# Optimization experiments

Hardware: AMD Instinct MI355X
Metric: run time of the kernel (lower is better)

Reference implementation:

```python
import jax, jax.numpy as jnp
import numpy as np

N_QUBITS = 10
N_GEN = 4
Q_DEPTH = 6
BATCH = 1024


def _cz_chain_diag(n):
    # Diagonal of the CZ chain CZ(0,1) CZ(1,2) ... CZ(n-2,n-1):
    # phase (-1)^(# adjacent 1-1 pairs) per computational basis state.
    idx = np.arange(2 ** n)
    bits = (idx[:, None] >> np.arange(n - 1, -1, -1)) & 1  # wire 0 = most significant (PennyLane)
    pairs = (bits[:, :-1] & bits[:, 1:]).sum(axis=1)
    return ((-1.0) ** pairs).astype(np.float32).reshape((2,) * n)

_CZ = jnp.asarray(_cz_chain_diag(N_QUBITS))


def _ry(t):
    c = jnp.cos(0.5 * t)
    s = jnp.sin(0.5 * t)
    return jnp.stack([jnp.stack([c, -s]), jnp.stack([s, c])]).astype(jnp.complex64)


def _rx(t):
    c = jnp.cos(0.5 * t).astype(jnp.complex64)
    js = (1j * jnp.sin(0.5 * t)).astype(jnp.complex64)
    return jnp.stack([jnp.stack([c, -js]), jnp.stack([-js, c])])


def _apply_1q(state, gate, wire):
    # state: (2,)*n complex statevector; apply 2x2 gate on `wire`.
    state = jnp.moveaxis(state, wire, -1)
    state = jnp.einsum('...j,ij->...i', state, gate)
    return jnp.moveaxis(state, -1, wire)


def _circuit(noise_s, weights, cz):
    # noise_s: (n_qubits,), weights: (q_depth, n_qubits)
    n = noise_s.shape[0]
    state = jnp.zeros((2,) * n, jnp.complex64).at[(0,) * n].set(1.0)
    for q in range(n):
        state = _apply_1q(state, _ry(noise_s[q]), q)
        state = _apply_1q(state, _rx(noise_s[q]), q)

    def layer(st, w):
        for q in range(n):
            st = _apply_1q(st, _ry(w[q]), q)
        return st * cz, None

    state, _ = jax.lax.scan(layer, state, weights)
    # <X_q> = Re <psi| X_q |psi>; X_q flips the q-th wire.
    return jnp.stack([jnp.real(jnp.vdot(state, jnp.flip(state, axis=q))) for q in range(n)])


def setup_inputs() -> dict:
    key = jax.random.key(0)
    k1, k2 = jax.random.split(key)
    noise = jax.random.normal(k1, (BATCH, N_QUBITS), dtype=jnp.float32)
    q_params = jax.random.uniform(k2, (N_GEN, Q_DEPTH, N_QUBITS), dtype=jnp.float32)  # q_delta=1.0 * rand
    return {"noise": noise, "q_params": q_params}


def reference(noise, q_params):
    per_sample = lambda ns, w: _circuit(ns, w, _CZ)
    per_gen = jax.vmap(lambda w: jax.vmap(lambda ns: per_sample(ns, w))(noise))(q_params)  # (G, B, n)
    out = jnp.transpose(per_gen, (1, 0, 2)).reshape(noise.shape[0], N_GEN * N_QUBITS)
    return out.astype(jnp.float32)
```

## Files before the change

### kernel.cpp

```cpp
#include <hip/hip_runtime.h>

#define NQ 10
#define NG 4
#define QD 6
#define NBATCH 1024
#define WPB 4


template<int CTRL, int RM, int BM, bool BC>
__device__ __forceinline__ float dppmov(float x) {
    return __int_as_float(__builtin_amdgcn_update_dpp(
        0, __float_as_int(x), CTRL, RM, BM, BC));
}

__device__ __forceinline__ float pxor1 (float x){ return dppmov<0xB1,0xF,0xF,false>(x); }
__device__ __forceinline__ float pxor2 (float x){ return dppmov<0x4E,0xF,0xF,false>(x); }
__device__ __forceinline__ float pxor4 (float x){
    return dppmov<0x1B,0xF,0xF,false>(dppmov<0x141,0xF,0xF,false>(x));
}
__device__ __forceinline__ float pxor8 (float x){
    return dppmov<0x141,0xF,0xF,false>(dppmov<0x140,0xF,0xF,false>(x));
}
__device__ __forceinline__ float pxor16(float x){ return __shfl_xor(x, 16, 64); }
__device__ __forceinline__ float pxor32(float x){ return __shfl_xor(x, 32, 64); }

struct PX1  { static __device__ __forceinline__ float f(float x){ return pxor1(x); } };
struct PX2  { static __device__ __forceinline__ float f(float x){ return pxor2(x); } };
struct PX4  { static __device__ __forceinline__ float f(float x){ return pxor4(x); } };
struct PX8  { static __device__ __forceinline__ float f(float x){ return pxor8(x); } };
struct PX16 { static __device__ __forceinline__ float f(float x){ return pxor16(x); } };
struct PX32 { static __device__ __forceinline__ float f(float x){ return pxor32(x); } };

__device__ __forceinline__ float wave_reduce(float x) {
    x += dppmov<0x111,0xF,0xF,true >(x);
    x += dppmov<0x112,0xF,0xF,true >(x);
    x += dppmov<0x114,0xF,0xF,true >(x);
    x += dppmov<0x118,0xF,0xF,true >(x);
    x += dppmov<0x142,0xA,0xF,false>(x);
    x += dppmov<0x143,0xC,0xF,false>(x);
    return __int_as_float(__builtin_amdgcn_readlane(__float_as_int(x), 63));
}

template<class PF, int LM>
__device__ __forceinline__ void cross_rot(float (&ar)[16], float (&ai)[16],
                                          float c, float s, int lane) {
    const float sgn = (lane & LM) ? s : -s;
#pragma unroll
    for (int j = 0; j < 16; ++j) {
        float pa = PF::f(ar[j]);
        float pb = PF::f(ai[j]);
        ar[j] = c * ar[j] + sgn * pa;
        ai[j] = c * ai[j] + sgn * pb;
    }
}

template<int M>
__device__ __forceinline__ void intra_rot(float (&ar)[16], float (&ai)[16],
                                          float c, float s) {
#pragma unroll
    for (int j = 0; j < 16; ++j) {
        if ((j & M) == 0) {
            const int k = j | M;
            float a0 = ar[j], a1 = ar[k];
            ar[j] = c * a0 - s * a1;
            ar[k] = s * a0 + c * a1;
            float b0 = ai[j], b1 = ai[k];
            ai[j] = c * b0 - s * b1;
            ai[k] = s * b0 + c * b1;
        }
    }
}

template<class PF>
__device__ __forceinline__ float cross_exp(const float (&ar)[16], const float (&ai)[16]) {
    float sum = 0.f;
#pragma unroll
    for (int j = 0; j < 16; ++j)
        sum += ar[j] * PF::f(ar[j]) + ai[j] * PF::f(ai[j]);
    return sum;
}

template<int M>
__device__ __forceinline__ float intra_exp(const float (&ar)[16], const float (&ai)[16]) {
    float sum = 0.f;
#pragma unroll
    for (int j = 0; j < 16; ++j)
        sum += ar[j] * ar[j ^ M] + ai[j] * ai[j ^ M];
    return sum;
}

__global__ __launch_bounds__(64 * WPB) void qsim_kernel(
    const float* __restrict__ noise,
    const float* __restrict__ qp,
    float* __restrict__ out)
{
    const int wave = threadIdx.x >> 6;
    const int lane = threadIdx.x & 63;
    const int g    = blockIdx.x & 3;
    const int b    = (blockIdx.x >> 2) * WPB + wave;

    float nc[NQ], ns[NQ];
#pragma unroll
    for (int q = 0; q < NQ; ++q) {
        float t = 0.5f * noise[b * NQ + q];
        __sincosf(t, &ns[q], &nc[q]);
    }

    float ar[16], ai[16];
    float hr = 1.f, hi = 0.f;
#pragma unroll
    for (int p = 4; p <= 9; ++p) {
        const int q = NQ - 1 - p;
        const int bit = (lane >> (p - 4)) & 1;
        float cc = nc[q], ss = ns[q];
        float gr, gi;
        if (bit) { gr = cc * ss; gi = -gr; }
        else     { gr = cc * cc; gi = -ss * ss; }
        float tr = hr * gr - hi * gi;
        float ti = hr * gi + hi * gr;
        hr = tr; hi = ti;
    }
#pragma unroll
    for (int j = 0; j < 16; ++j) {
        float r = hr, im = hi;
#pragma unroll
        for (int p = 0; p < 4; ++p) {
            const int q = NQ - 1 - p;
            float cc = nc[q], ss = ns[q];
            float gr, gi;
            if ((j >> p) & 1) { gr = cc * ss; gi = -gr; }
            else              { gr = cc * cc; gi = -ss * ss; }
            float tr = r * gr - im * gi;
            float ti = r * gi + im * gr;
            r = tr; im = ti;
        }
        ar[j] = r; ai[j] = im;
    }

    float czs[16];
#pragma unroll
    for (int j = 0; j < 16; ++j) {
        unsigned i = ((unsigned)lane << 4) | (unsigned)j;
        czs[j] = (__popc(i & (i >> 1)) & 1) ? -1.f : 1.f;
    }

    const float* w = qp + g * (QD * NQ);
#pragma unroll 1
    for (int l = 0; l < QD; ++l) {
        float c[NQ], sn[NQ];
#pragma unroll
        for (int q = 0; q < NQ; ++q)
            __sincosf(0.5f * w[l * NQ + q], &sn[q], &c[q]);

        cross_rot<PX32,32>(ar, ai, c[0], sn[0], lane);
        cross_rot<PX16,16>(ar, ai, c[1], sn[1], lane);
        cross_rot<PX8 , 8>(ar, ai, c[2], sn[2], lane);
        cross_rot<PX4 , 4>(ar, ai, c[3], sn[3], lane);
        cross_rot<PX2 , 2>(ar, ai, c[4], sn[4], lane);
        cross_rot<PX1 , 1>(ar, ai, c[5], sn[5], lane);
        intra_rot<8>(ar, ai, c[6], sn[6]);
        intra_rot<4>(ar, ai, c[7], sn[7]);
        intra_rot<2>(ar, ai, c[8], sn[8]);
        intra_rot<1>(ar, ai, c[9], sn[9]);

#pragma unroll
        for (int j = 0; j < 16; ++j) { ar[j] *= czs[j]; ai[j] *= czs[j]; }
    }

    float outval = 0.f;
    {
        float s0 = wave_reduce(cross_exp<PX32>(ar, ai)); outval = (lane == 0) ? s0 : outval;
        float s1 = wave_reduce(cross_exp<PX16>(ar, ai)); outval = (lane == 1) ? s1 : outval;
        float s2 = wave_reduce(cross_exp<PX8 >(ar, ai)); outval = (lane == 2) ? s2 : outval;
        float s3 = wave_reduce(cross_exp<PX4 >(ar, ai)); outval = (lane == 3) ? s3 : outval;
        float s4 = wave_reduce(cross_exp<PX2 >(ar, ai)); outval = (lane == 4) ? s4 : outval;
        float s5 = wave_reduce(cross_exp<PX1 >(ar, ai)); outval = (lane == 5) ? s5 : outval;
        float s6 = wave_reduce(intra_exp<8>(ar, ai));    outval = (lane == 6) ? s6 : outval;
        float s7 = wave_reduce(intra_exp<4>(ar, ai));    outval = (lane == 7) ? s7 : outval;
        float s8 = wave_reduce(intra_exp<2>(ar, ai));    outval = (lane == 8) ? s8 : outval;
        float s9 = wave_reduce(intra_exp<1>(ar, ai));    outval = (lane == 9) ? s9 : outval;
    }

    if (lane < NQ)
        out[b * (NG * NQ) + g * NQ + lane] = outval;
}

extern "C" void kernel_launch(void* const* d_in, const int* in_sizes, int n_in,
                              void* d_out, int out_size, void* d_ws, size_t ws_size,
                              hipStream_t stream) {
    const float* noise = (const float*)d_in[0];
    const float* qp    = (const float*)d_in[1];
    float* out = (float*)d_out;

    const int nblocks = (NBATCH * NG) / WPB;
    qsim_kernel<<<nblocks, 64 * WPB, 0, stream>>>(noise, qp, out);
}
```

Baseline: 99.61 us.

## Pack complex amplitudes into float2 vectors, swizzle xor16, factor initial state

Stores each amplitude as a float2 vector so the compiler can emit packed FP32 ops (v_pk_fma/v_pk_mul) for the rotations, CZ phase and expectation sums. The lane-xor-16 exchange moves from a bpermute-based shuffle to ds_swizzle. Initial product-state construction is factored into shared partial products. The aim is fewer VALU instructions per gate, with some risk that the packed code is not generated or that register pressure rises.

```diff
diff --git a/kernel.cpp b/kernel.cpp
--- a/kernel.cpp
+++ b/kernel.cpp
@@ -7,29 +7,32 @@
 #define WPB 4
 
 
+typedef float v2f __attribute__((ext_vector_type(2)));
+
 template<int CTRL, int RM, int BM, bool BC>
 __device__ __forceinline__ float dppmov(float x) {
     return __int_as_float(__builtin_amdgcn_update_dpp(
         0, __float_as_int(x), CTRL, RM, BM, BC));
 }
 
-__device__ __forceinline__ float pxor1 (float x){ return dppmov<0xB1,0xF,0xF,false>(x); }
-__device__ __forceinline__ float pxor2 (float x){ return dppmov<0x4E,0xF,0xF,false>(x); }
-__device__ __forceinline__ float pxor4 (float x){
-    return dppmov<0x1B,0xF,0xF,false>(dppmov<0x141,0xF,0xF,false>(x));
+template<int CTRL>
+__device__ __forceinline__ v2f dpp2(v2f x) {
+    v2f r;
+    r.x = dppmov<CTRL,0xF,0xF,false>(x.x);
+    r.y = dppmov<CTRL,0xF,0xF,false>(x.y);
+    return r;
 }
-__device__ __forceinline__ float pxor8 (float x){
-    return dppmov<0x141,0xF,0xF,false>(dppmov<0x140,0xF,0xF,false>(x));
+
+__device__ __forceinline__ float swz16(float x) {
+    return __int_as_float(__builtin_amdgcn_ds_swizzle(__float_as_int(x), 0x401F));
 }
-__device__ __forceinline__ float pxor16(float x){ return __shfl_xor(x, 16, 64); }
-__device__ __forceinline__ float pxor32(float x){ return __shfl_xor(x, 32, 64); }
 
-struct PX1  { static __device__ __forceinline__ float f(float x){ return pxor1(x); } };
-struct PX2  { static __device__ __forceinline__ float f(float x){ return pxor2(x); } };
-struct PX4  { static __device__ __forceinline__ float f(float x){ return pxor4(x); } };
-struct PX8  { static __device__ __forceinline__ float f(float x){ return pxor8(x); } };
-struct PX16 { static __device__ __forceinline__ float f(float x){ return pxor16(x); } };
-struct PX32 { static __device__ __forceinline__ float f(float x){ return pxor32(x); } };
+struct PX1  { static __device__ __forceinline__ v2f f(v2f x){ return dpp2<0xB1>(x); } };
+struct PX2  { static __device__ __forceinline__ v2f f(v2f x){ return dpp2<0x4E>(x); } };
+struct PX4  { static __device__ __forceinline__ v2f f(v2f x){ return dpp2<0x1B>(dpp2<0x141>(x)); } };
+struct PX8  { static __device__ __forceinline__ v2f f(v2f x){ return dpp2<0x141>(dpp2<0x140>(x)); } };
+struct PX16 { static __device__ __forceinline__ v2f f(v2f x){ v2f r; r.x = swz16(x.x); r.y = swz16(x.y); return r; } };
+struct PX32 { static __device__ __forceinline__ v2f f(v2f x){ v2f r; r.x = __shfl_xor(x.x, 32, 64); r.y = __shfl_xor(x.y, 32, 64); return r; } };
 
 __device__ __forceinline__ float wave_reduce(float x) {
     x += dppmov<0x111,0xF,0xF,true >(x);
@@ -41,52 +44,54 @@
     return __int_as_float(__builtin_amdgcn_readlane(__float_as_int(x), 63));
 }
 
+__device__ __forceinline__ v2f cmul(v2f a, v2f b) {
+    v2f r;
+    r.x = a.x * b.x - a.y * b.y;
+    r.y = a.x * b.y + a.y * b.x;
+    return r;
+}
+
 template<class PF, int LM>
-__device__ __forceinline__ void cross_rot(float (&ar)[16], float (&ai)[16],
-                                          float c, float s, int lane) {
-    const float sgn = (lane & LM) ? s : -s;
+__device__ __forceinline__ void cross_rot(v2f (&s)[16], float c, float sn, int lane) {
+    const float sgn = (lane & LM) ? sn : -sn;
 #pragma unroll
     for (int j = 0; j < 16; ++j) {
-        float pa = PF::f(ar[j]);
-        float pb = PF::f(ai[j]);
-        ar[j] = c * ar[j] + sgn * pa;
-        ai[j] = c * ai[j] + sgn * pb;
+        v2f p = PF::f(s[j]);
+        s[j] = c * s[j] + sgn * p;
     }
 }
 
 template<int M>
-__device__ __forceinline__ void intra_rot(float (&ar)[16], float (&ai)[16],
-                                          float c, float s) {
+__device__ __forceinline__ void intra_rot(v2f (&s)[16], float c, float sn) {
 #pragma unroll
     for (int j = 0; j < 16; ++j) {
         if ((j & M) == 0) {
             const int k = j | M;
-            float a0 = ar[j], a1 = ar[k];
-            ar[j] = c * a0 - s * a1;
-            ar[k] = s * a0 + c * a1;
-            float b0 = ai[j], b1 = ai[k];
-            ai[j] = c * b0 - s * b1;
-            ai[k] = s * b0 + c * b1;
+            v2f v0 = s[j], v1 = s[k];
+            s[j] = c * v0 - sn * v1;
+            s[k] = sn * v0 + c * v1;
         }
     }
 }
 
 template<class PF>
-__device__ __forceinline__ float cross_exp(const float (&ar)[16], const float (&ai)[16]) {
-    float sum = 0.f;
+__device__ __forceinline__ float cross_exp(const v2f (&s)[16]) {
+    v2f acc = {0.f, 0.f};
 #pragma unroll
-    for (int j = 0; j < 16; ++j)
-        sum += ar[j] * PF::f(ar[j]) + ai[j] * PF::f(ai[j]);
-    return sum;
+    for (int j = 0; j < 16; ++j) {
+        v2f p = PF::f(s[j]);
+        acc += s[j] * p;
+    }
+    return acc.x + acc.y;
 }
 
 template<int M>
-__device__ __forceinline__ float intra_exp(const float (&ar)[16], const float (&ai)[16]) {
-    float sum = 0.f;
+__device__ __forceinline__ float intra_exp(const v2f (&s)[16]) {
+    v2f acc = {0.f, 0.f};
 #pragma unroll
     for (int j = 0; j < 16; ++j)
-        sum += ar[j] * ar[j ^ M] + ai[j] * ai[j ^ M];
-    return sum;
+        acc += s[j] * s[j ^ M];
+    return acc.x + acc.y;
 }
 
 __global__ __launch_bounds__(64 * WPB) void qsim_kernel(
@@ -106,35 +111,32 @@
         __sincosf(t, &ns[q], &nc[q]);
     }
 
-    float ar[16], ai[16];
-    float hr = 1.f, hi = 0.f;
+    auto fac = [&](int q, int bit) -> v2f {
+        float cc = nc[q], ss = ns[q];
+        v2f r;
+        if (bit) { r.x = cc * ss; r.y = -r.x; }
+        else     { r.x = cc * cc; r.y = -ss * ss; }
+        return r;
+    };
+
+    v2f h = {1.f, 0.f};
 #pragma unroll
-    for (int p = 4; p <= 9; ++p) {
-        const int q = NQ - 1 - p;
-        const int bit = (lane >> (p - 4)) & 1;
-        float cc = nc[q], ss = ns[q];
-        float gr, gi;
-        if (bit) { gr = cc * ss; gi = -gr; }
-        else     { gr = cc * cc; gi = -ss * ss; }
-        float tr = hr * gr - hi * gi;
-        float ti = hr * gi + hi * gr;
-        hr = tr; hi = ti;
-    }
+    for (int p = 4; p <= 9; ++p)
+        h = cmul(h, fac(NQ - 1 - p, (lane >> (p - 4)) & 1));
+
+    v2f s[16];
+    {
+        v2f t01[4], t23[4];
 #pragma unroll
-    for (int j = 0; j < 16; ++j) {
-        float r = hr, im = hi;
+        for (int a = 0; a < 4; ++a) {
+            t01[a] = cmul(fac(9, a & 1), fac(8, (a >> 1) & 1));
+            t23[a] = cmul(fac(7, a & 1), fac(6, (a >> 1) & 1));
+        }
+        v2f pre[4];
 #pragma unroll
-        for (int p = 0; p < 4; ++p) {
-            const int q = NQ - 1 - p;
-            float cc = nc[q], ss = ns[q];
-            float gr, gi;
-            if ((j >> p) & 1) { gr = cc * ss; gi = -gr; }
-            else              { gr = cc * cc; gi = -ss * ss; }
-            float tr = r * gr - im * gi;
-            float ti = r * gi + im * gr;
-            r = tr; im = ti;
-        }
-        ar[j] = r; ai[j] = im;
+        for (int a = 0; a < 4; ++a) pre[a] = cmul(h, t01[a]);
+#pragma unroll
+        for (int j = 0; j < 16; ++j) s[j] = cmul(pre[j & 3], t23[j >> 2]);
     }
 
     float czs[16];
@@ -152,33 +154,33 @@
         for (int q = 0; q < NQ; ++q)
             __sincosf(0.5f * w[l * NQ + q], &sn[q], &c[q]);
 
-        cross_rot<PX32,32>(ar, ai, c[0], sn[0], lane);
-        cross_rot<PX16,16>(ar, ai, c[1], sn[1], lane);
-        cross_rot<PX8 , 8>(ar, ai, c[2], sn[2], lane);
-        cross_rot<PX4 , 4>(ar, ai, c[3], sn[3], lane);
-        cross_rot<PX2 , 2>(ar, ai, c[4], sn[4], lane);
-        cross_rot<PX1 , 1>(ar, ai, c[5], sn[5], lane);
-        intra_rot<8>(ar, ai, c[6], sn[6]);
-        intra_rot<4>(ar, ai, c[7], sn[7]);
-        intra_rot<2>(ar, ai, c[8], sn[8]);
-        intra_rot<1>(ar, ai, c[9], sn[9]);
+        cross_rot<PX32,32>(s, c[0], sn[0], lane);
+        cross_rot<PX16,16>(s, c[1], sn[1], lane);
+        cross_rot<PX8 , 8>(s, c[2], sn[2], lane);
+        cross_rot<PX4 , 4>(s, c[3], sn[3], lane);
+        cross_rot<PX2 , 2>(s, c[4], sn[4], lane);
+        cross_rot<PX1 , 1>(s, c[5], sn[5], lane);
+        intra_rot<8>(s, c[6], sn[6]);
+        intra_rot<4>(s, c[7], sn[7]);
+        intra_rot<2>(s, c[8], sn[8]);
+        intra_rot<1>(s, c[9], sn[9]);
 
 #pragma unroll
-        for (int j = 0; j < 16; ++j) { ar[j] *= czs[j]; ai[j] *= czs[j]; }
+        for (int j = 0; j < 16; ++j) s[j] *= czs[j];
     }
 
     float outval = 0.f;
     {
-        float s0 = wave_reduce(cross_exp<PX32>(ar, ai)); outval = (lane == 0) ? s0 : outval;
-        float s1 = wave_reduce(cross_exp<PX16>(ar, ai)); outval = (lane == 1) ? s1 : outval;
-        float s2 = wave_reduce(cross_exp<PX8 >(ar, ai)); outval = (lane == 2) ? s2 : outval;
-        float s3 = wave_reduce(cross_exp<PX4 >(ar, ai)); outval = (lane == 3) ? s3 : outval;
-        float s4 = wave_reduce(cross_exp<PX2 >(ar, ai)); outval = (lane == 4) ? s4 : outval;
-        float s5 = wave_reduce(cross_exp<PX1 >(ar, ai)); outval = (lane == 5) ? s5 : outval;
-        float s6 = wave_reduce(intra_exp<8>(ar, ai));    outval = (lane == 6) ? s6 : outval;
-        float s7 = wave_reduce(intra_exp<4>(ar, ai));    outval = (lane == 7) ? s7 : outval;
-        float s8 = wave_reduce(intra_exp<2>(ar, ai));    outval = (lane == 8) ? s8 : outval;
-        float s9 = wave_reduce(intra_exp<1>(ar, ai));    outval = (lane == 9) ? s9 : outval;
+        float s0 = wave_reduce(cross_exp<PX32>(s)); outval = (lane == 0) ? s0 : outval;
+        float s1 = wave_reduce(cross_exp<PX16>(s)); outval = (lane == 1) ? s1 : outval;
+        float s2 = wave_reduce(cross_exp<PX8 >(s)); outval = (lane == 2) ? s2 : outval;
+        float s3 = wave_reduce(cross_exp<PX4 >(s)); outval = (lane == 3) ? s3 : outval;
+        float s4 = wave_reduce(cross_exp<PX2 >(s)); outval = (lane == 4) ? s4 : outval;
+        float s5 = wave_reduce(cross_exp<PX1 >(s)); outval = (lane == 5) ? s5 : outval;
+        float s6 = wave_reduce(intra_exp<8>(s));    outval = (lane == 6) ? s6 : outval;
+        float s7 = wave_reduce(intra_exp<4>(s));    outval = (lane == 7) ? s7 : outval;
+        float s8 = wave_reduce(intra_exp<2>(s));    outval = (lane == 8) ? s8 : outval;
+        float s9 = wave_reduce(intra_exp<1>(s));    outval = (lane == 9) ? s9 : outval;
     }
 
     if (lane < NQ)
```

Result: faster. 97.11 us (-2.5%).
